# Kernel tuning notes

Hardware: AMD Instinct MI355X
Metric: run time of the kernel (lower is better)

Reference implementation:

```python
import jax, jax.numpy as jnp
import numpy as np

GRID = 10
NV = 6
SD = 4
TSD = NV * SD  # 24
PRED = 5
DT = 0.1
BN_EPS = 1e-5


def _conv(x, w, b):
    y = jax.lax.conv_general_dilated(x, w, (1, 1), 'SAME',
                                     dimension_numbers=('NCHW', 'OIHW', 'NCHW'))
    return y + b[None, :, None, None]


def _pool(x):
    return jax.lax.reduce_window(x, -jnp.inf, jax.lax.max,
                                 (1, 1, 2, 2), (1, 1, 2, 2), 'VALID')


def _bn_eval(x, g, b):
    # eval-mode BatchNorm with running_mean=0, running_var=1
    return g * x / jnp.sqrt(1.0 + BN_EPS) + b


def _lstm(x, Wih, Whh, bih, bhh):
    # x: [B, T, D]; torch gate order i, f, g, o
    B = x.shape[0]
    H = Whh.shape[1]
    def step(carry, xt):
        h, c = carry
        gates = xt @ Wih.T + h @ Whh.T + bih + bhh
        i, f, g, o = jnp.split(gates, 4, axis=-1)
        c = jax.nn.sigmoid(f) * c + jax.nn.sigmoid(i) * jnp.tanh(g)
        h = jax.nn.sigmoid(o) * jnp.tanh(c)
        return (h, c), h
    init = (jnp.zeros((B, H), x.dtype), jnp.zeros((B, H), x.dtype))
    (h, c), ys = jax.lax.scan(step, init, jnp.swapaxes(x, 0, 1))
    return jnp.swapaxes(ys, 0, 1), (h, c)


def setup_inputs() -> dict:
    key = jax.random.key(0)
    B, T, D = 512, 100, 400
    C = D // (GRID * GRID)  # 4
    H = 32
    ks = iter(jax.random.split(key, 64))
    r = lambda shape, s=0.1: (s * jax.random.normal(next(ks), shape)).astype(jnp.float32)
    inp = {
        'observations': jax.random.normal(next(ks), (B, T, D), dtype=jnp.float32),
        # CNN
        'c1w': r((16, C, 3, 3)), 'c1b': r((16,)),
        'c2w': r((32, 16, 3, 3)), 'c2b': r((32,)),
        # FCN  (cnn_output_size = 32 * 2 * 2 = 128)
        'f1w': r((128, 128)), 'f1b': r((128,)),
        'bn1g': jnp.ones((128,), jnp.float32), 'bn1b': jnp.zeros((128,), jnp.float32),
        'f2w': r((64, 128)), 'f2b': r((64,)),
        'bn2g': jnp.ones((64,), jnp.float32), 'bn2b': jnp.zeros((64,), jnp.float32),
        # encoder / decoder LSTMs
        'eWih': r((4 * H, 64)), 'eWhh': r((4 * H, H)), 'ebih': r((4 * H,)), 'ebhh': r((4 * H,)),
        'dWih': r((4 * H, H)), 'dWhh': r((4 * H, H)), 'dbih': r((4 * H,)), 'dbhh': r((4 * H,)),
        'ow': r((2 * NV, H)), 'ob': r((2 * NV,)),
        # filter-layer noise LSTMs + FCs
        'qWih': r((4 * H, TSD)), 'qWhh': r((4 * H, H)), 'qbih': r((4 * H,)), 'qbhh': r((4 * H,)),
        'qfw': r((TSD, H)), 'qfb': r((TSD,)),
        'rWih': r((4 * H, TSD)), 'rWhh': r((4 * H, H)), 'rbih': r((4 * H,)), 'rbhh': r((4 * H,)),
        'rfw': r((TSD, H)), 'rfb': r((TSD,)),
    }
    return inp


def _forward(observations, c1w, c1b, c2w, c2b, f1w, f1b, bn1g, bn1b, f2w, f2b,
             bn2g, bn2b, eWih, eWhh, ebih, ebhh, dWih, dWhh, dbih, dbhh, ow, ob,
             qWih, qWhh, qbih, qbhh, qfw, qfb, rWih, rWhh, rbih, rbhh, rfw, rfb):
    B, T, D = observations.shape
    C = c1w.shape[1]
    # ---- InteractionLayer: CNN over all timesteps at once ----
    x = observations.reshape(B * T, C, GRID, GRID)
    x = _pool(jax.nn.relu(_conv(x, c1w, c1b)))   # [B*T,16,5,5]
    x = _pool(jax.nn.relu(_conv(x, c2w, c2b)))   # [B*T,32,2,2]
    x = x.reshape(B * T, -1)                      # [B*T,128]
    x = jax.nn.relu(_bn_eval(x @ f1w.T + f1b, bn1g, bn1b))
    x = jax.nn.relu(_bn_eval(x @ f2w.T + f2b, bn2g, bn2b))  # [B*T,64]
    feats = x.reshape(B, T, 64)
    enc_out, (dh, dc) = _lstm(feats, eWih, eWhh, ebih, ebhh)
    din = enc_out[:, -1]
    preds = []
    for _ in range(PRED):
        gates = din @ dWih.T + dh @ dWhh.T + dbih + dbhh
        i, f, g, o = jnp.split(gates, 4, axis=-1)
        dc = jax.nn.sigmoid(f) * dc + jax.nn.sigmoid(i) * jnp.tanh(g)
        dh = jax.nn.sigmoid(o) * jnp.tanh(dc)
        preds.append(dh @ ow.T + ob)
        din = dh
    accel = jnp.stack(preds, axis=1)  # [B, PRED, 2*NV]
    # ---- MotionLayer (closed-form cumsum kinematics) ----
    init_state = observations[:, -1, :4]
    a = accel.reshape(B, PRED, NV, 2)
    v0 = jnp.zeros((B, NV, 2), jnp.float32).at[:, 0].set(init_state[:, 2:4])
    p0 = jnp.zeros((B, NV, 2), jnp.float32).at[:, 0].set(init_state[:, :2])
    v = v0[:, None] + DT * jnp.cumsum(a, axis=1)
    disp = v * DT + 0.5 * a * DT * DT
    p = p0[:, None] + jnp.cumsum(disp, axis=1)
    traj = jnp.concatenate([p, v], axis=-1).reshape(B, PRED, TSD)
    # ---- FilterLayer: learned noise + Kalman scan ----
    qo, _ = _lstm(traj, qWih, qWhh, qbih, qbhh)
    Qm = jax.vmap(jnp.diag)(jnp.abs(qo[:, -1] @ qfw.T + qfb))  # [B,24,24]
    ro, _ = _lstm(traj, rWih, rWhh, rbih, rbhh)
    Rm = jax.vmap(jnp.diag)(jnp.abs(ro[:, -1] @ rfw.T + rfb))
    Fb = jnp.array([[1, 0, DT, 0], [0, 1, 0, DT], [0, 0, 1, 0], [0, 0, 0, 1]], jnp.float32)
    Fm = jnp.kron(jnp.eye(NV, dtype=jnp.float32), Fb)  # [24,24]
    I = jnp.eye(TSD, dtype=jnp.float32)
    s0 = jnp.zeros((B, TSD), jnp.float32).at[:, :4].set(init_state)
    P0 = jnp.broadcast_to(I, (B, TSD, TSD)) + jnp.zeros((B, TSD, TSD), jnp.float32)
    def kf_step(carry, z):
        s, P = carry
        s_m = s @ Fm.T
        P_m = jnp.einsum('ij,bjk,lk->bil', Fm, P, Fm) + Qm
        S = P_m + Rm
        Kt = jnp.linalg.solve(S, jnp.swapaxes(P_m, 1, 2))
        K = jnp.swapaxes(Kt, 1, 2)
        s_new = s_m + jnp.einsum('bij,bj->bi', K, z - s_m)
        P_new = jnp.einsum('bij,bjk->bik', I - K, P_m)
        return (s_new, P_new), s_new
    _, filt = jax.lax.scan(kf_step, (s0, P0), jnp.swapaxes(traj, 0, 1))
    return jnp.swapaxes(filt, 0, 1)  # [B, PRED, 24]


def reference(observations, c1w, c1b, c2w, c2b, f1w, f1b, bn1g, bn1b, f2w, f2b,
              bn2g, bn2b, eWih, eWhh, ebih, ebhh, dWih, dWhh, dbih, dbhh, ow, ob,
              qWih, qWhh, qbih, qbhh, qfw, qfb, rWih, rWhh, rbih, rbhh, rfw, rfb):
    return _forward(observations, c1w, c1b, c2w, c2b, f1w, f1b, bn1g, bn1b,
                    f2w, f2b, bn2g, bn2b, eWih, eWhh, ebih, ebhh, dWih, dWhh,
                    dbih, dbhh, ow, ob, qWih, qWhh, qbih, qbhh, qfw, qfb,
                    rWih, rWhh, rbih, rbhh, rfw, rfb)
```

## Files before the change

### kernel.cpp

```cpp
#include <hip/hip_runtime.h>

#define BT 51200
#define NB 512

#define P1_OFF   ((size_t)0)
#define X_OFF    ((size_t)20480000)
#define GX_OFF   ((size_t)0)

__device__ __forceinline__ float sigf(float x) {
  return __fdividef(1.f, 1.f + __expf(-x));
}
__device__ __forceinline__ float tanhf2(float x) {
  float ax = fabsf(x);
  float e = __expf(-2.f * ax);
  float r = __fdividef(1.f - e, 1.f + e);
  return x < 0.f ? -r : r;
}

__global__ __attribute__((amdgpu_flat_work_group_size(1024, 1024)))
__attribute__((amdgpu_waves_per_eu(4, 4)))
void k1_conv1(const float* __restrict__ obs, const float* __restrict__ w,
              const float* __restrict__ bias, float* __restrict__ p1) {
  __shared__ float xs[64 * 401];
  int tid = threadIdx.x;
  int i0 = blockIdx.x * 64;
  for (int idx = tid; idx < 25600; idx += 1024) {
    int item = idx / 400, feat = idx - item * 400;
    xs[item * 401 + feat] = obs[(size_t)(i0 + item) * 400 + feat];
  }
  __syncthreads();
  int lane = tid & 63;
  int wv = __builtin_amdgcn_readfirstlane(tid >> 6);
  const float* xrow = xs + lane * 401;

#define LOADR(R, C, RR) do { \
  int r_ = 2 * p - 1 + (RR); \
  R[0] = 0.f; R[11] = 0.f; \
  if (r_ >= 0 && r_ <= 9) { \
    _Pragma("unroll") \
    for (int j = 0; j < 10; ++j) R[j + 1] = xrow[(C) * 100 + r_ * 10 + j]; \
  } else { \
    _Pragma("unroll") \
    for (int j = 0; j < 10; ++j) R[j + 1] = 0.f; \
  } \
} while (0)

#define FMAU(II, RA, RB, RC, C) do { \
  const float* wa_ = w + wv * 36 + (C) * 9; \
  _Pragma("unroll") \
  for (int q = 0; q < 5; ++q) { \
    _Pragma("unroll") \
    for (int jj = 0; jj < 2; ++jj) { \
      int cb = 2 * q + jj; \
      acc[q][II][jj] += RA[cb] * wa_[0] + RA[cb + 1] * wa_[1] + RA[cb + 2] * wa_[2] \
                      + RB[cb] * wa_[3] + RB[cb + 1] * wa_[4] + RB[cb + 2] * wa_[5] \
                      + RC[cb] * wa_[6] + RC[cb + 1] * wa_[7] + RC[cb + 2] * wa_[8]; \
    } \
  } \
} while (0)

  float b0 = bias[wv];

#pragma unroll 1
  for (int p = 0; p < 5; ++p) {
    float acc[5][2][2];
#pragma unroll
    for (int q = 0; q < 5; ++q)
#pragma unroll
      for (int ii = 0; ii < 2; ++ii)
#pragma unroll
        for (int jj = 0; jj < 2; ++jj) acc[q][ii][jj] = b0;
    float R0[12], R1[12], R2[12], R3[12], R4[12], R5[12];
    LOADR(R0, 0, 0); LOADR(R1, 0, 1); LOADR(R2, 0, 2);
    LOADR(R3, 0, 3); LOADR(R4, 1, 0);
    FMAU(0, R0, R1, R2, 0);
    LOADR(R5, 1, 1); LOADR(R0, 1, 2);
    FMAU(1, R1, R2, R3, 0);
    LOADR(R1, 1, 3); LOADR(R2, 2, 0);
    FMAU(0, R4, R5, R0, 1);
    LOADR(R3, 2, 1); LOADR(R4, 2, 2);
    FMAU(1, R5, R0, R1, 1);
    LOADR(R5, 2, 3); LOADR(R0, 3, 0);
    FMAU(0, R2, R3, R4, 2);
    LOADR(R1, 3, 1); LOADR(R2, 3, 2);
    FMAU(1, R3, R4, R5, 2);
    LOADR(R3, 3, 3);
    FMAU(0, R0, R1, R2, 3);
    FMAU(1, R1, R2, R3, 3);
#pragma unroll
    for (int q = 0; q < 5; ++q) {
      float m = fmaxf(fmaxf(acc[q][0][0], acc[q][0][1]),
                      fmaxf(acc[q][1][0], acc[q][1][1]));
      m = fmaxf(m, 0.f);
      p1[(size_t)(wv * 25 + p * 5 + q) * BT + i0 + lane] = m;
    }
  }
#undef LOADR
#undef FMAU
}

__global__ __launch_bounds__(256, 2)
void k2_conv2(const float* __restrict__ p1, const float* __restrict__ w,
              const float* __restrict__ bias, float* __restrict__ x) {
  int bid = blockIdx.x;
  int inner = bid >> 3;
  int oc = inner & 3;
  int g = ((inner >> 2) << 3) | (bid & 7);
  int item = g * 256 + threadIdx.x;
  float acc[8][16];
#pragma unroll
  for (int o = 0; o < 8; ++o) {
    float bv = bias[oc * 8 + o];
#pragma unroll
    for (int pos = 0; pos < 16; ++pos) acc[o][pos] = bv;
  }
#pragma unroll 1
  for (int c = 0; c < 16; ++c) {
    float in[6][6];
#pragma unroll
    for (int t = 0; t < 6; ++t) { in[0][t] = 0.f; in[t][0] = 0.f; }
#pragma unroll
    for (int i = 0; i < 5; ++i)
#pragma unroll
      for (int j = 0; j < 5; ++j)
        in[i + 1][j + 1] = p1[(size_t)(c * 25 + i * 5 + j) * BT + item];
#pragma unroll
    for (int o = 0; o < 8; ++o) {
#pragma unroll
      for (int i = 0; i < 4; ++i)
#pragma unroll
        for (int j = 0; j < 4; ++j) {
          float a = acc[o][i * 4 + j];
#pragma unroll
          for (int dr = 0; dr < 3; ++dr)
#pragma unroll
            for (int dj = 0; dj < 3; ++dj)
              a += in[i + dr][j + dj] * w[((oc * 8 + o) * 16 + c) * 9 + dr * 3 + dj];
          acc[o][i * 4 + j] = a;
        }
    }
  }
#pragma unroll
  for (int o = 0; o < 8; ++o)
#pragma unroll
    for (int p = 0; p < 2; ++p)
#pragma unroll
      for (int q = 0; q < 2; ++q) {
        float m = fmaxf(fmaxf(acc[o][(2 * p) * 4 + 2 * q], acc[o][(2 * p) * 4 + 2 * q + 1]),
                        fmaxf(acc[o][(2 * p + 1) * 4 + 2 * q], acc[o][(2 * p + 1) * 4 + 2 * q + 1]));
        m = fmaxf(m, 0.f);
        x[(size_t)((oc * 8 + o) * 4 + p * 2 + q) * BT + item] = m;
      }
}

__global__ __launch_bounds__(256, 2)
void k3_fc(const float* __restrict__ x,
           const float* __restrict__ f1w, const float* __restrict__ f1b,
           const float* __restrict__ bn1g, const float* __restrict__ bn1b,
           const float* __restrict__ f2w, const float* __restrict__ f2b,
           const float* __restrict__ bn2g, const float* __restrict__ bn2b,
           const float* __restrict__ eWih, const float* __restrict__ ebih,
           const float* __restrict__ ebhh, float* __restrict__ gx) {
  __shared__ float xs[128 * 64];
  __shared__ float ys[128 * 64];
  const float BNRS = 0.9999950000374997f;
  int tid = threadIdx.x;
  int lane = tid & 63;
  int wv = __builtin_amdgcn_readfirstlane(tid >> 6);
  int i0 = blockIdx.x * 64;
#pragma unroll
  for (int r = 0; r < 32; ++r) {
    int k = r * 4 + (tid >> 6);
    xs[k * 64 + lane] = x[(size_t)k * BT + i0 + lane];
  }
  __syncthreads();
#pragma unroll 1
  for (int jj = 0; jj < 8; ++jj) {
    int j0 = wv * 32 + jj * 4;
    float a[4] = {0.f, 0.f, 0.f, 0.f};
#pragma unroll 8
    for (int k = 0; k < 128; ++k) {
      float xv = xs[k * 64 + lane];
#pragma unroll
      for (int u = 0; u < 4; ++u) a[u] += xv * f1w[(j0 + u) * 128 + k];
    }
#pragma unroll
    for (int u = 0; u < 4; ++u) {
      int j = j0 + u;
      float v = a[u] + f1b[j];
      v = bn1g[j] * v * BNRS + bn1b[j];
      ys[j * 64 + lane] = fmaxf(v, 0.f);
    }
  }
  __syncthreads();
#pragma unroll 1
  for (int jj = 0; jj < 4; ++jj) {
    int j0 = wv * 16 + jj * 4;
    float a[4] = {0.f, 0.f, 0.f, 0.f};
#pragma unroll 8
    for (int k = 0; k < 128; ++k) {
      float yv = ys[k * 64 + lane];
#pragma unroll
      for (int u = 0; u < 4; ++u) a[u] += yv * f2w[(j0 + u) * 128 + k];
    }
#pragma unroll
    for (int u = 0; u < 4; ++u) {
      int j = j0 + u;
      float v = a[u] + f2b[j];
      v = bn2g[j] * v * BNRS + bn2b[j];
      xs[j * 64 + lane] = fmaxf(v, 0.f);
    }
  }
  __syncthreads();
#pragma unroll 1
  for (int jj = 0; jj < 8; ++jj) {
    int j0 = wv * 32 + jj * 4;
    float a[4] = {0.f, 0.f, 0.f, 0.f};
#pragma unroll 8
    for (int k = 0; k < 64; ++k) {
      float zv = xs[k * 64 + lane];
#pragma unroll
      for (int u = 0; u < 4; ++u) a[u] += zv * eWih[(j0 + u) * 64 + k];
    }
#pragma unroll
    for (int u = 0; u < 4; ++u) {
      int j = j0 + u;
      gx[(size_t)j * BT + i0 + lane] = a[u] + ebih[j] + ebhh[j];
    }
  }
}

__global__ __launch_bounds__(128, 2)
void k456(const float* __restrict__ obs, const float* __restrict__ gx,
          const float* __restrict__ eWhh,
          const float* __restrict__ dWih, const float* __restrict__ dWhh,
          const float* __restrict__ dbih, const float* __restrict__ dbhh,
          const float* __restrict__ ow, const float* __restrict__ ob,
          const float* __restrict__ qWih, const float* __restrict__ qWhh,
          const float* __restrict__ qbih, const float* __restrict__ qbhh,
          const float* __restrict__ qfw, const float* __restrict__ qfb,
          const float* __restrict__ rWih, const float* __restrict__ rWhh,
          const float* __restrict__ rbih, const float* __restrict__ rbhh,
          const float* __restrict__ rfw, const float* __restrict__ rfb,
          float* __restrict__ out) {
  __shared__ float arena[8064];
  __shared__ float tL2[2 * 120];
  int tid = threadIdx.x;
  int lane = tid & 63, w = tid >> 6;
  int b = blockIdx.x * 2 + w;
  float* tL = tL2 + w * 120;
  int xl = (lane & 31) + 32;
  int l12 = lane < 12 ? lane : 0;
  int l24 = lane < 24 ? lane : 0;

  for (int idx = tid; idx < 4096; idx += 128) {
    int g = idx & 127, k = idx >> 7;
    arena[k * 128 + g] = eWhh[g * 32 + k];
  }
  __syncthreads();
  float cc = 0.f, hh = 0.f;
  size_t base0 = (size_t)b * 100;
  float ga_n = gx[(size_t)lane * BT + base0];
  float gb_n = gx[(size_t)(lane + 64) * BT + base0];
#pragma unroll 1
  for (int t = 0; t < 100; ++t) {
    float ga = ga_n, gb2 = gb_n;
    if (t < 99) {
      ga_n = gx[(size_t)lane * BT + base0 + t + 1];
      gb_n = gx[(size_t)(lane + 64) * BT + base0 + t + 1];
    }
#pragma unroll
    for (int k = 0; k < 32; ++k) {
      float hk = __shfl(hh, k);
      ga += hk * arena[k * 128 + lane];
      gb2 += hk * arena[k * 128 + lane + 64];
    }
    float gaX = __shfl(ga, xl);
    float gbX = __shfl(gb2, xl);
    if (lane < 32) {
      float ig = sigf(ga), fg = sigf(gaX);
      float gg = tanhf2(gb2), og = sigf(gbX);
      cc = fg * cc + ig * gg;
      hh = og * tanhf2(cc);
    }
  }

  __syncthreads();
  for (int idx = tid; idx < 4096; idx += 128) {
    int k = idx >> 7, g = idx & 127;
    arena[idx] = dWih[g * 32 + k] + dWhh[g * 32 + k];
  }
  for (int idx = tid; idx < 384; idx += 128) {
    int k = idx / 12, j = idx - k * 12;
    arena[4096 + idx] = ow[j * 32 + k];
  }
  for (int idx = tid; idx < 128; idx += 128)
    arena[4480 + idx] = dbih[idx] + dbhh[idx];
  __syncthreads();
  {
    const float* dwT = arena;
    const float* owT = arena + 4096;
    const float* dbs = arena + 4480;
    float aReg[5];
#pragma unroll 1
    for (int s = 0; s < 5; ++s) {
      float ga = dbs[lane], gb2 = dbs[lane + 64];
#pragma unroll
      for (int k = 0; k < 32; ++k) {
        float hk = __shfl(hh, k);
        ga += hk * dwT[k * 128 + lane];
        gb2 += hk * dwT[k * 128 + lane + 64];
      }
      float gaX = __shfl(ga, xl);
      float gbX = __shfl(gb2, xl);
      if (lane < 32) {
        float ig = sigf(ga), fg = sigf(gaX);
        float gg = tanhf2(gb2), og = sigf(gbX);
        cc = fg * cc + ig * gg;
        hh = og * tanhf2(cc);
      }
      float pa = ob[l12];
#pragma unroll
      for (int k = 0; k < 32; ++k) pa += __shfl(hh, k) * owT[k * 12 + l12];
      aReg[s] = pa;
    }
    if (lane < 12) {
      int n = lane >> 1, d = lane & 1;
      float v0 = 0.f, p0 = 0.f;
      if (n == 0) {
        p0 = obs[(size_t)b * 40000 + 39600 + d];
        v0 = obs[(size_t)b * 40000 + 39600 + 2 + d];
      }
      float vc = v0, pc = p0;
#pragma unroll
      for (int s = 0; s < 5; ++s) {
        float a = aReg[s];
        vc += 0.1f * a;
        pc += vc * 0.1f + a * 0.005f;
        tL[s * 24 + n * 4 + d] = pc;
        tL[s * 24 + n * 4 + 2 + d] = vc;
      }
    }
  }

  float qdiag = 0.f, rdiag = 0.f;
#pragma unroll 1
  for (int qr = 0; qr < 2; ++qr) {
    __syncthreads();
    const float* Wih = qr ? rWih : qWih;
    const float* Whh = qr ? rWhh : qWhh;
    const float* bih = qr ? rbih : qbih;
    const float* bhh = qr ? rbhh : qbhh;
    const float* fw  = qr ? rfw  : qfw;
    const float* fb  = qr ? rfb  : qfb;
    for (int idx = tid; idx < 3072; idx += 128) {
      int k = idx >> 7, g = idx & 127;
      arena[idx] = Wih[g * 24 + k];
    }
    for (int idx = tid; idx < 4096; idx += 128) {
      int k = idx >> 7, g = idx & 127;
      arena[3072 + idx] = Whh[g * 32 + k];
    }
    for (int idx = tid; idx < 768; idx += 128) {
      int k = idx / 24, j = idx - k * 24;
      arena[7168 + idx] = fw[j * 32 + k];
    }
    for (int idx = tid; idx < 128; idx += 128)
      arena[7936 + idx] = bih[idx] + bhh[idx];
    __syncthreads();
    const float* ihT = arena;
    const float* hhT = arena + 3072;
    const float* fwT = arena + 7168;
    const float* bs  = arena + 7936;
    hh = 0.f;
    cc = 0.f;
#pragma unroll 1
    for (int s = 0; s < 5; ++s) {
      float ga = bs[lane], gb2 = bs[lane + 64];
#pragma unroll
      for (int k = 0; k < 24; ++k) {
        float z = tL[s * 24 + k];
        ga += z * ihT[k * 128 + lane];
        gb2 += z * ihT[k * 128 + lane + 64];
      }
#pragma unroll
      for (int k = 0; k < 32; ++k) {
        float hk = __shfl(hh, k);
        ga += hk * hhT[k * 128 + lane];
        gb2 += hk * hhT[k * 128 + lane + 64];
      }
      float gaX = __shfl(ga, xl);
      float gbX = __shfl(gb2, xl);
      if (lane < 32) {
        float ig = sigf(ga), fg = sigf(gaX);
        float gg = tanhf2(gb2), og = sigf(gbX);
        cc = fg * cc + ig * gg;
        hh = og * tanhf2(cc);
      }
    }
    float qv = fb[l24];
#pragma unroll
    for (int k = 0; k < 32; ++k) qv += __shfl(hh, k) * fwT[k * 24 + l24];
    if (qr == 0) qdiag = fabsf(qv); else rdiag = fabsf(qv);
  }

  {
    float sv = 0.f, qv = 0.f, rv = 0.f;
    if (lane < 24) {
      sv = (lane < 4) ? obs[(size_t)b * 40000 + 39600 + lane] : 0.f;
      qv = qdiag;
      rv = rdiag;
    }
    float p[24];
#pragma unroll
    for (int i = 0; i < 24; ++i) p[i] = (i == lane) ? 1.f : 0.f;
    const int srcPF = ((lane & 3) < 2) ? (lane + 2) : lane;
    const int srcA = (lane < 24) ? lane : (lane - 24);
#pragma unroll 1
    for (int s = 0; s < 5; ++s) {
      float sshift = __shfl(sv, srcPF);
      float smv = sv + (((lane & 3) < 2) ? 0.1f * sshift : 0.f);
#pragma unroll
      for (int i = 0; i < 24; ++i)
        if ((i & 3) < 2) p[i] += 0.1f * p[i + 2];
#pragma unroll
      for (int i = 0; i < 24; ++i) {
        float t = __shfl(p[i], srcPF);
        if ((lane & 3) < 2) p[i] += 0.1f * t;
      }
#pragma unroll
      for (int i = 0; i < 24; ++i) p[i] += (i == lane) ? qv : 0.f;
      float a[24];
#pragma unroll
      for (int i = 0; i < 24; ++i) {
        float t = __shfl(p[i], srcA);
        a[i] = (lane < 24) ? (p[i] + ((i == lane) ? rv : 0.f)) : t;
      }
#pragma unroll
      for (int k = 0; k < 24; ++k) {
        float piv = __shfl(a[k], k);
        float inv = 1.f / piv;
        float t = a[k] * inv;
#pragma unroll
        for (int i = 0; i < 24; ++i) {
          if (i != k) {
            float fi = __shfl(a[i], k);
            a[i] = fmaf(-fi, t, a[i]);
          }
        }
        a[k] = t;
      }
      float zv = tL[s * 24 + l24];
      float innv = zv - smv;
      float acc = 0.f;
#pragma unroll
      for (int m = 0; m < 24; ++m) acc += a[m] * __shfl(innv, m);
      float kupd = __shfl(acc, 24 + l24);
      sv = smv + kupd;
      if (lane < 24) out[(size_t)b * 120 + s * 24 + lane] = sv;
      float pn[24];
#pragma unroll
      for (int i = 0; i < 24; ++i) {
        float acc2 = 0.f;
#pragma unroll
        for (int k = 0; k < 24; ++k) acc2 += __shfl(a[k], 24 + i) * p[k];
        pn[i] = p[i] - acc2;
      }
#pragma unroll
      for (int i = 0; i < 24; ++i) p[i] = pn[i];
    }
  }
}

extern "C" void kernel_launch(void* const* d_in, const int* in_sizes, int n_in,
                              void* d_out, int out_size, void* d_ws, size_t ws_size,
                              hipStream_t stream) {
  (void)in_sizes; (void)n_in; (void)out_size; (void)ws_size;
  const float* obs  = (const float*)d_in[0];
  const float* c1w  = (const float*)d_in[1];
  const float* c1b  = (const float*)d_in[2];
  const float* c2w  = (const float*)d_in[3];
  const float* c2b  = (const float*)d_in[4];
  const float* f1w  = (const float*)d_in[5];
  const float* f1b  = (const float*)d_in[6];
  const float* bn1g = (const float*)d_in[7];
  const float* bn1b = (const float*)d_in[8];
  const float* f2w  = (const float*)d_in[9];
  const float* f2b  = (const float*)d_in[10];
  const float* bn2g = (const float*)d_in[11];
  const float* bn2b = (const float*)d_in[12];
  const float* eWih = (const float*)d_in[13];
  const float* eWhh = (const float*)d_in[14];
  const float* ebih = (const float*)d_in[15];
  const float* ebhh = (const float*)d_in[16];
  const float* dWih = (const float*)d_in[17];
  const float* dWhh = (const float*)d_in[18];
  const float* dbih = (const float*)d_in[19];
  const float* dbhh = (const float*)d_in[20];
  const float* ow   = (const float*)d_in[21];
  const float* ob   = (const float*)d_in[22];
  const float* qWih = (const float*)d_in[23];
  const float* qWhh = (const float*)d_in[24];
  const float* qbih = (const float*)d_in[25];
  const float* qbhh = (const float*)d_in[26];
  const float* qfw  = (const float*)d_in[27];
  const float* qfb  = (const float*)d_in[28];
  const float* rWih = (const float*)d_in[29];
  const float* rWhh = (const float*)d_in[30];
  const float* rbih = (const float*)d_in[31];
  const float* rbhh = (const float*)d_in[32];
  const float* rfw  = (const float*)d_in[33];
  const float* rfb  = (const float*)d_in[34];

  float* ws = (float*)d_ws;
  float* p1   = ws + P1_OFF;
  float* x    = ws + X_OFF;
  float* gx   = ws + GX_OFF;
  float* out  = (float*)d_out;

  k1_conv1<<<800, 1024, 0, stream>>>(obs, c1w, c1b, p1);
  k2_conv2<<<800, 256, 0, stream>>>(p1, c2w, c2b, x);
  k3_fc<<<800, 256, 0, stream>>>(x, f1w, f1b, bn1g, bn1b, f2w, f2b, bn2g, bn2b,
                                 eWih, ebih, ebhh, gx);
  k456<<<256, 128, 0, stream>>>(obs, gx, eWhh,
                                dWih, dWhh, dbih, dbhh, ow, ob,
                                qWih, qWhh, qbih, qbhh, qfw, qfb,
                                rWih, rWhh, rbih, rbhh, rfw, rfb,
                                out);
}
```

Before: 700.0 us.

## Halve conv1 block tile, stage weights in LDS, vectorize observation loads

The first conv kernel now runs 1600 blocks of 512 threads, each covering 32 items, instead of 800 blocks of 1024 threads covering 64 items. Each wave now handles two output channels split across half-waves. The block index is remapped so paired half-tiles stay adjacent. Observations load through float4 global reads, and the 16x36 conv weights are staged in shared memory and held in registers per channel. The goal is to halve LDS per block for better occupancy, widen global loads, and drop repeated global weight reads, at the cost of per-lane weight loads and 32-wide store segments for p1.

```diff
diff --git a/kernel.cpp b/kernel.cpp
--- a/kernel.cpp
+++ b/kernel.cpp
@@ -17,21 +17,31 @@
   return x < 0.f ? -r : r;
 }
 
-__global__ __attribute__((amdgpu_flat_work_group_size(1024, 1024)))
-__attribute__((amdgpu_waves_per_eu(4, 4)))
+__global__ __launch_bounds__(512, 4)
 void k1_conv1(const float* __restrict__ obs, const float* __restrict__ w,
               const float* __restrict__ bias, float* __restrict__ p1) {
-  __shared__ float xs[64 * 401];
+  __shared__ float xs[32 * 401];
+  __shared__ float wsh[16 * 36];
   int tid = threadIdx.x;
-  int i0 = blockIdx.x * 64;
-  for (int idx = tid; idx < 25600; idx += 1024) {
-    int item = idx / 400, feat = idx - item * 400;
-    xs[item * 401 + feat] = obs[(size_t)(i0 + item) * 400 + feat];
-  }
+  int phys = blockIdx.x;
+  int x8 = phys & 7;
+  int rest = phys >> 3;
+  int half = rest & 1;
+  int pair = (rest >> 1) * 8 + x8;
+  int i0 = pair * 64 + half * 32;
+  for (int idx = tid; idx < 3200; idx += 512) {
+    int item = idx / 100, f = idx - item * 100;
+    float4 v = ((const float4*)obs)[(size_t)(i0 + item) * 100 + f];
+    float* d = xs + item * 401 + f * 4;
+    d[0] = v.x; d[1] = v.y; d[2] = v.z; d[3] = v.w;
+  }
+  for (int idx = tid; idx < 576; idx += 512) wsh[idx] = w[idx];
   __syncthreads();
   int lane = tid & 63;
   int wv = __builtin_amdgcn_readfirstlane(tid >> 6);
-  const float* xrow = xs + lane * 401;
+  int item = lane & 31;
+  int oc = wv * 2 + (lane >> 5);
+  const float* xrow = xs + item * 401;
 
 #define LOADR(R, C, RR) do { \
   int r_ = 2 * p - 1 + (RR); \
@@ -46,20 +56,23 @@
 } while (0)
 
 #define FMAU(II, RA, RB, RC, C) do { \
-  const float* wa_ = w + wv * 36 + (C) * 9; \
+  const float* wp_ = wsh + oc * 36 + (C) * 9; \
+  float w0_ = wp_[0], w1_ = wp_[1], w2_ = wp_[2]; \
+  float w3_ = wp_[3], w4_ = wp_[4], w5_ = wp_[5]; \
+  float w6_ = wp_[6], w7_ = wp_[7], w8_ = wp_[8]; \
   _Pragma("unroll") \
   for (int q = 0; q < 5; ++q) { \
     _Pragma("unroll") \
     for (int jj = 0; jj < 2; ++jj) { \
       int cb = 2 * q + jj; \
-      acc[q][II][jj] += RA[cb] * wa_[0] + RA[cb + 1] * wa_[1] + RA[cb + 2] * wa_[2] \
-                      + RB[cb] * wa_[3] + RB[cb + 1] * wa_[4] + RB[cb + 2] * wa_[5] \
-                      + RC[cb] * wa_[6] + RC[cb + 1] * wa_[7] + RC[cb + 2] * wa_[8]; \
+      acc[q][II][jj] += RA[cb] * w0_ + RA[cb + 1] * w1_ + RA[cb + 2] * w2_ \
+                      + RB[cb] * w3_ + RB[cb + 1] * w4_ + RB[cb + 2] * w5_ \
+                      + RC[cb] * w6_ + RC[cb + 1] * w7_ + RC[cb + 2] * w8_; \
     } \
   } \
 } while (0)
 
-  float b0 = bias[wv];
+  float b0 = bias[oc];
 
 #pragma unroll 1
   for (int p = 0; p < 5; ++p) {
@@ -92,7 +105,7 @@
       float m = fmaxf(fmaxf(acc[q][0][0], acc[q][0][1]),
                       fmaxf(acc[q][1][0], acc[q][1][1]));
       m = fmaxf(m, 0.f);
-      p1[(size_t)(wv * 25 + p * 5 + q) * BT + i0 + lane] = m;
+      p1[(size_t)(oc * 25 + p * 5 + q) * BT + i0 + item] = m;
     }
   }
 #undef LOADR
@@ -518,7 +531,7 @@
   float* gx   = ws + GX_OFF;
   float* out  = (float*)d_out;
 
-  k1_conv1<<<800, 1024, 0, stream>>>(obs, c1w, c1b, p1);
+  k1_conv1<<<1600, 512, 0, stream>>>(obs, c1w, c1b, p1);
   k2_conv2<<<800, 256, 0, stream>>>(p1, c2w, c2b, x);
   k3_fc<<<800, 256, 0, stream>>>(x, f1w, f1b, bn1g, bn1b, f2w, f2b, bn2g, bn2b,
                                  eWih, ebih, ebhh, gx);
```

After: 1.131 ms. 1.62x slower.

## Add conv1 variant with 32-item, 512-thread blocks and LDS-staged weights

Applied to the files above, without the earlier changes.

Adds an alternative conv1 kernel that processes 32 items per block with 512 threads, maps two output channels per wave (half-wave per channel), stages the conv weights in LDS, and remaps block indices so adjacent physical blocks cover interleaved 32-item halves. The launch picks this variant at runtime only if the compiled kernel uses at least 100 registers, otherwise it falls back to the original kernel. The intent is to relax the 1024-thread/4-waves constraint so the compiler can keep more registers, and to cut redundant global weight loads. The runtime attribute query adds a one-time host cost and makes the chosen path depend on compiler register allocation.

```diff
diff --git a/kernel.cpp b/kernel.cpp
--- a/kernel.cpp
+++ b/kernel.cpp
@@ -17,10 +17,101 @@
   return x < 0.f ? -r : r;
 }
 
+__global__ __launch_bounds__(512, 1)
+void k1_conv1_exp(const float* __restrict__ obs, const float* __restrict__ w,
+                  const float* __restrict__ bias, float* __restrict__ p1) {
+  __shared__ float xs[32 * 411];
+  __shared__ float wsh[16 * 36];
+  int tid = threadIdx.x;
+  int phys = blockIdx.x;
+  int x8 = phys & 7;
+  int rest = phys >> 3;
+  int half = rest & 1;
+  int pair = (rest >> 1) * 8 + x8;
+  int i0 = pair * 64 + half * 32;
+  for (int idx = tid; idx < 12800; idx += 512) {
+    int item = idx / 400, feat = idx - item * 400;
+    xs[item * 411 + feat] = obs[(size_t)(i0 + item) * 400 + feat];
+  }
+  for (int idx = tid; idx < 576; idx += 512) wsh[idx] = w[idx];
+  __syncthreads();
+  int lane = tid & 63;
+  int item = lane & 31;
+  int oc = (tid >> 6) * 2 + (lane >> 5);
+  const float* xrow = xs + item * 411;
+
+#define LOADR(R, C, RR) do { \
+  int r_ = 2 * p - 1 + (RR); \
+  R[0] = 0.f; R[11] = 0.f; \
+  if (r_ >= 0 && r_ <= 9) { \
+    _Pragma("unroll") \
+    for (int j = 0; j < 10; ++j) R[j + 1] = xrow[(C) * 100 + r_ * 10 + j]; \
+  } else { \
+    _Pragma("unroll") \
+    for (int j = 0; j < 10; ++j) R[j + 1] = 0.f; \
+  } \
+} while (0)
+
+#define FMAU(II, RA, RB, RC, C) do { \
+  const float* wp_ = wsh + oc * 36 + (C) * 9; \
+  float w0_ = wp_[0], w1_ = wp_[1], w2_ = wp_[2]; \
+  float w3_ = wp_[3], w4_ = wp_[4], w5_ = wp_[5]; \
+  float w6_ = wp_[6], w7_ = wp_[7], w8_ = wp_[8]; \
+  _Pragma("unroll") \
+  for (int q = 0; q < 5; ++q) { \
+    _Pragma("unroll") \
+    for (int jj = 0; jj < 2; ++jj) { \
+      int cb = 2 * q + jj; \
+      acc[q][II][jj] += RA[cb] * w0_ + RA[cb + 1] * w1_ + RA[cb + 2] * w2_ \
+                      + RB[cb] * w3_ + RB[cb + 1] * w4_ + RB[cb + 2] * w5_ \
+                      + RC[cb] * w6_ + RC[cb + 1] * w7_ + RC[cb + 2] * w8_; \
+    } \
+  } \
+} while (0)
+
+  float b0 = bias[oc];
+#pragma unroll 1
+  for (int p = 0; p < 5; ++p) {
+    float acc[5][2][2];
+#pragma unroll
+    for (int q = 0; q < 5; ++q)
+#pragma unroll
+      for (int ii = 0; ii < 2; ++ii)
+#pragma unroll
+        for (int jj = 0; jj < 2; ++jj) acc[q][ii][jj] = b0;
+    float R0[12], R1[12], R2[12], R3[12], R4[12], R5[12];
+    LOADR(R0, 0, 0); LOADR(R1, 0, 1); LOADR(R2, 0, 2);
+    LOADR(R3, 0, 3); LOADR(R4, 1, 0);
+    FMAU(0, R0, R1, R2, 0);
+    LOADR(R5, 1, 1); LOADR(R0, 1, 2);
+    FMAU(1, R1, R2, R3, 0);
+    LOADR(R1, 1, 3); LOADR(R2, 2, 0);
+    FMAU(0, R4, R5, R0, 1);
+    LOADR(R3, 2, 1); LOADR(R4, 2, 2);
+    FMAU(1, R5, R0, R1, 1);
+    LOADR(R5, 2, 3); LOADR(R0, 3, 0);
+    FMAU(0, R2, R3, R4, 2);
+    LOADR(R1, 3, 1); LOADR(R2, 3, 2);
+    FMAU(1, R3, R4, R5, 2);
+    LOADR(R3, 3, 3);
+    FMAU(0, R0, R1, R2, 3);
+    FMAU(1, R1, R2, R3, 3);
+#pragma unroll
+    for (int q = 0; q < 5; ++q) {
+      float m = fmaxf(fmaxf(acc[q][0][0], acc[q][0][1]),
+                      fmaxf(acc[q][1][0], acc[q][1][1]));
+      m = fmaxf(m, 0.f);
+      p1[(size_t)(oc * 25 + p * 5 + q) * BT + i0 + item] = m;
+    }
+  }
+#undef LOADR
+#undef FMAU
+}
+
 __global__ __attribute__((amdgpu_flat_work_group_size(1024, 1024)))
 __attribute__((amdgpu_waves_per_eu(4, 4)))
-void k1_conv1(const float* __restrict__ obs, const float* __restrict__ w,
-              const float* __restrict__ bias, float* __restrict__ p1) {
+void k1_conv1_big(const float* __restrict__ obs, const float* __restrict__ w,
+                  const float* __restrict__ bias, float* __restrict__ p1) {
   __shared__ float xs[64 * 401];
   int tid = threadIdx.x;
   int i0 = blockIdx.x * 64;
@@ -60,7 +151,6 @@
 } while (0)
 
   float b0 = bias[wv];
-
 #pragma unroll 1
   for (int p = 0; p < 5; ++p) {
     float acc[5][2][2];
@@ -518,7 +608,17 @@
   float* gx   = ws + GX_OFF;
   float* out  = (float*)d_out;
 
-  k1_conv1<<<800, 1024, 0, stream>>>(obs, c1w, c1b, p1);
+  static int k1_use_exp = -1;
+  if (k1_use_exp < 0) {
+    hipFuncAttributes attr;
+    hipError_t e = hipFuncGetAttributes(&attr, (const void*)k1_conv1_exp);
+    k1_use_exp = (e == hipSuccess && attr.numRegs >= 100) ? 1 : 0;
+  }
+  if (k1_use_exp)
+    k1_conv1_exp<<<1600, 512, 0, stream>>>(obs, c1w, c1b, p1);
+  else
+    k1_conv1_big<<<800, 1024, 0, stream>>>(obs, c1w, c1b, p1);
+
   k2_conv2<<<800, 256, 0, stream>>>(p1, c2w, c2b, x);
   k3_fc<<<800, 256, 0, stream>>>(x, f1w, f1b, bn1g, bn1b, f2w, f2b, bn2g, bn2b,
                                  eWih, ebih, ebhh, gx);
```

Measured after the change: 678.5 us. 3.1% less time.
